# Kernel optimization log

Measured on AMD Instinct MI355X. Metric: run time of the kernel, lower is better.

## Reference

```python
import jax, jax.numpy as jnp
import numpy as np

B, T, I, H = 64, 2048, 64, 256


def setup_inputs() -> dict:
    key = jax.random.key(0)
    ks = jax.random.split(key, 7)
    s_ih = 1.0 / np.sqrt(H)
    return {
        "x": jax.random.normal(ks[0], (B, T, I), dtype=jnp.float32),
        "W_ih": jax.random.normal(ks[1], (H, I), dtype=jnp.float32) * s_ih,
        "W_hh": jax.random.normal(ks[2], (H, H), dtype=jnp.float32) * s_ih,
        "b_ih": jax.random.normal(ks[3], (H,), dtype=jnp.float32) * s_ih,
        "b_hh": jax.random.normal(ks[4], (H,), dtype=jnp.float32) * s_ih,
        "W_fc": jax.random.normal(ks[5], (1, H), dtype=jnp.float32) * s_ih,
        "b_fc": jax.random.normal(ks[6], (1,), dtype=jnp.float32) * s_ih,
    }


def reference(x, W_ih, W_hh, b_ih, b_hh, W_fc, b_fc):
    # Precompute input projection for all timesteps: [B,T,H]
    pre = jnp.einsum('bti,hi->bth', x, W_ih) + b_ih + b_hh
    pre_t = jnp.swapaxes(pre, 0, 1)  # [T,B,H]

    def step(h, p_t):
        h_new = jnp.tanh(p_t + h @ W_hh.T)
        return h_new, h_new

    h0 = jnp.zeros((x.shape[0], W_hh.shape[0]), dtype=x.dtype)
    _, hs = jax.lax.scan(step, h0, pre_t)  # hs: [T,B,H]
    out = jnp.swapaxes(hs, 0, 1)  # [B,T,H]
    return out @ W_fc.T + b_fc  # [B,T,1]
```

## Files before the change

### kernel.cpp

```cpp
#include <hip/hip_runtime.h>

#define BB 64
#define TT 2048
#define II 64
#define HH 256

typedef __fp16 h2_t __attribute__((ext_vector_type(2)));
typedef __fp16 h8_t __attribute__((ext_vector_type(8)));

#define H2(i) __builtin_bit_cast(h2_t, (i))
#define I32(h) __builtin_bit_cast(int, (h))

#if __has_builtin(__builtin_amdgcn_fdot2)
#define FDOT2(a, b, c) __builtin_amdgcn_fdot2((a), (b), (c), false)
#else
__device__ __forceinline__ float FDOT2(h2_t a, h2_t b, float c) {
    return fmaf((float)a[0], (float)b[0], fmaf((float)a[1], (float)b[1], c));
}
#endif

__device__ __forceinline__ float ftanh(float x) {
    float e = __expf(2.0f * x);
    return 1.0f - 2.0f * __builtin_amdgcn_rcpf(e + 1.0f);
}

template <int CTRL>
__device__ __forceinline__ float dpp_add(float v) {
    int s = __builtin_amdgcn_update_dpp(0, __float_as_int(v), CTRL, 0xF, 0xF, true);
    return v + __int_as_float(s);
}
template <int CTRL>
__device__ __forceinline__ float dpp_get(float v) {
    int s = __builtin_amdgcn_update_dpp(0, __float_as_int(v), CTRL, 0xF, 0xF, true);
    return __int_as_float(s);
}
template <int PAT>
__device__ __forceinline__ float swz_get(float v) {
    return __int_as_float(__builtin_amdgcn_ds_swizzle(__float_as_int(v), PAT));
}

__device__ __forceinline__ float mrg4(float a, float b, int lane) {
    float t = (lane & 4) ? b : a;
    float u = (lane & 4) ? a : b;
    return t + swz_get<0x101F>(u);
}
__device__ __forceinline__ float mrg2(float a, float b, int lane) {
    float t = (lane & 2) ? b : a;
    float u = (lane & 2) ? a : b;
    return t + dpp_get<0x4E>(u);
}
__device__ __forceinline__ float mrg1(float a, float b, int lane) {
    float t = (lane & 1) ? b : a;
    float u = (lane & 1) ? a : b;
    return t + dpp_get<0xB1>(u);
}

__launch_bounds__(256, 1)
__global__ void rnn_fused(const float* __restrict__ x,
                          const float* __restrict__ W_ih,
                          const float* __restrict__ W_hh,
                          const float* __restrict__ b_ih,
                          const float* __restrict__ b_hh,
                          const float* __restrict__ W_fc,
                          const float* __restrict__ b_fc,
                          float* __restrict__ out) {
    __shared__ __align__(16) __fp16 hbuf[2][320];
    __shared__ float part[TT + 1][8];

    const int tid  = threadIdx.x;
    const int b    = blockIdx.x;
    const int lane = tid & 63;
    const int w    = tid >> 6;
    const int o    = lane >> 3;
    const int q    = lane & 7;

    int whh_i[8][16];
    int wih_i[8][4];
#pragma unroll
    for (int r = 0; r < 8; ++r) {
        const int t_r = w * 64 + o * 8 + r;
        const float4* wr = (const float4*)(W_hh + t_r * HH + q * 32);
#pragma unroll
        for (int jv = 0; jv < 8; ++jv) {
            const float4 wv = wr[jv];
            whh_i[r][jv * 2 + 0] = I32(__builtin_amdgcn_cvt_pkrtz(wv.x, wv.y));
            whh_i[r][jv * 2 + 1] = I32(__builtin_amdgcn_cvt_pkrtz(wv.z, wv.w));
        }
        const float4* wi = (const float4*)(W_ih + t_r * II + q * 8);
        const float4 wa = wi[0], wb = wi[1];
        wih_i[r][0] = I32(__builtin_amdgcn_cvt_pkrtz(wa.x, wa.y));
        wih_i[r][1] = I32(__builtin_amdgcn_cvt_pkrtz(wa.z, wa.w));
        wih_i[r][2] = I32(__builtin_amdgcn_cvt_pkrtz(wb.x, wb.y));
        wih_i[r][3] = I32(__builtin_amdgcn_cvt_pkrtz(wb.z, wb.w));
    }
#pragma unroll
    for (int j = 0; j < 128; ++j) asm volatile("" : "+v"(((int*)whh_i)[j]));
#pragma unroll
    for (int j = 0; j < 32; ++j) asm volatile("" : "+v"(((int*)wih_i)[j]));

    const int myrow = w * 64 + lane;
    const float bias = b_ih[myrow] + b_hh[myrow];
    const float wfc  = W_fc[myrow];
    const float bfc  = b_fc[0];

    for (int idx = tid; idx < 2 * 320; idx += 256) ((__fp16*)hbuf)[idx] = (__fp16)0.0f;
    __syncthreads();

    const float* xbase = x + (size_t)b * TT * II + q * 8;
    float* outb = out + (size_t)b * TT;

    const int hoff = (w * 2 + (lane >> 5)) * 80 + (lane & 31) * 2;
    __fp16* hw0 = (__fp16*)((char*)&hbuf[0][0] + hoff);
    __fp16* hw1 = (__fp16*)((char*)&hbuf[1][0] + hoff);
    const h8_t* hp0 = (const h8_t*)((const char*)&hbuf[0][0] + q * 80);
    const h8_t* hp1 = (const h8_t*)((const char*)&hbuf[1][0] + q * 80);

    h2_t xc[4];
    float4 sAa, sAc, sBa, sBc;
    {
        const float4* xp = (const float4*)(xbase);
        const float4 a = xp[0], c = xp[1];
        xc[0] = __builtin_amdgcn_cvt_pkrtz(a.x, a.y);
        xc[1] = __builtin_amdgcn_cvt_pkrtz(a.z, a.w);
        xc[2] = __builtin_amdgcn_cvt_pkrtz(c.x, c.y);
        xc[3] = __builtin_amdgcn_cvt_pkrtz(c.z, c.w);
        const float4* x1 = (const float4*)(xbase + II);
        sAa = x1[0]; sAc = x1[1];
        const float4* x2 = (const float4*)(xbase + 2 * II);
        sBa = x2[0]; sBc = x2[1];
    }

    float hn_prev = 0.0f;

#define STEP(IDX, HPIN, HWOUT, SA, SC)                                         \
    {                                                                          \
          \
        const h8_t hv0 = (HPIN)[0], hv1 = (HPIN)[1];                           \
        const h8_t hv2 = (HPIN)[2], hv3 = (HPIN)[3];                           \
           \
        {                                                                      \
            float c = hn_prev * wfc;                                           \
            c = dpp_add<0xB1>(c);                                      \
            c = dpp_add<0x4E>(c);                                      \
            c = dpp_add<0x141>(c);                \
            c = dpp_add<0x140>(c);                     \
            c = dpp_add<0x142>(c);    \
            if ((lane & 31) == 16) part[IDX][w * 2 + (lane >> 5)] = c;         \
        }                                                                      \
                 \
        float a0 = 0, a1 = 0, a2 = 0, a3 = 0, a4 = 0, a5 = 0, a6 = 0, a7 = 0;  \
        _Pragma("unroll")                                                      \
        for (int jv = 0; jv < 4; ++jv) {                                       \
            const h8_t hv = (jv == 0) ? hv0 : (jv == 1) ? hv1                  \
                          : (jv == 2) ? hv2 : hv3;                             \
            _Pragma("unroll")                                                  \
            for (int e = 0; e < 4; ++e) {                                      \
                const h2_t he = (e == 0) ? __builtin_shufflevector(hv, hv, 0, 1) \
                              : (e == 1) ? __builtin_shufflevector(hv, hv, 2, 3) \
                              : (e == 2) ? __builtin_shufflevector(hv, hv, 4, 5) \
                                         : __builtin_shufflevector(hv, hv, 6, 7); \
                const int j = jv * 4 + e;                                      \
                a0 = FDOT2(H2(whh_i[0][j]), he, a0);                           \
                a1 = FDOT2(H2(whh_i[1][j]), he, a1);                           \
                a2 = FDOT2(H2(whh_i[2][j]), he, a2);                           \
                a3 = FDOT2(H2(whh_i[3][j]), he, a3);                           \
                a4 = FDOT2(H2(whh_i[4][j]), he, a4);                           \
                a5 = FDOT2(H2(whh_i[5][j]), he, a5);                           \
                a6 = FDOT2(H2(whh_i[6][j]), he, a6);                           \
                a7 = FDOT2(H2(whh_i[7][j]), he, a7);                           \
            }                                                                  \
        }                                                                      \
        _Pragma("unroll")                                                      \
        for (int e = 0; e < 4; ++e) {                                          \
            a0 = FDOT2(H2(wih_i[0][e]), xc[e], a0);                            \
            a1 = FDOT2(H2(wih_i[1][e]), xc[e], a1);                            \
            a2 = FDOT2(H2(wih_i[2][e]), xc[e], a2);                            \
            a3 = FDOT2(H2(wih_i[3][e]), xc[e], a3);                            \
            a4 = FDOT2(H2(wih_i[4][e]), xc[e], a4);                            \
            a5 = FDOT2(H2(wih_i[5][e]), xc[e], a5);                            \
            a6 = FDOT2(H2(wih_i[6][e]), xc[e], a6);                            \
            a7 = FDOT2(H2(wih_i[7][e]), xc[e], a7);                            \
        }                                                                      \
         \
        xc[0] = __builtin_amdgcn_cvt_pkrtz((SA).x, (SA).y);                    \
        xc[1] = __builtin_amdgcn_cvt_pkrtz((SA).z, (SA).w);                    \
        xc[2] = __builtin_amdgcn_cvt_pkrtz((SC).x, (SC).y);                    \
        xc[3] = __builtin_amdgcn_cvt_pkrtz((SC).z, (SC).w);                    \
        {                                                                      \
            const int rn = ((IDX) + 3 < TT) ? ((IDX) + 3) : (TT - 1);          \
            const float4* xp = (const float4*)(xbase + rn * II);               \
            (SA) = xp[0]; (SC) = xp[1];                                        \
        }                                                                      \
         \
        const float A0 = mrg4(a0, a4, lane);                                   \
        const float A1 = mrg4(a1, a5, lane);                                   \
        const float A2 = mrg4(a2, a6, lane);                                   \
        const float A3 = mrg4(a3, a7, lane);                                   \
        const float B0 = mrg2(A0, A2, lane);                                   \
        const float B1 = mrg2(A1, A3, lane);                                   \
        const float C0 = mrg1(B0, B1, lane);                                   \
        const float hn = ftanh(C0 + bias);                                     \
        (HWOUT)[0] = (__fp16)hn;                                               \
        hn_prev = hn;                                                          \
           \
                             \
        asm volatile("s_waitcnt lgkmcnt(0)\n\ts_barrier" ::: "memory");        \
    }

    for (int ib = 0; ib < TT; ib += 2) {
        STEP(ib, hp0, hw1, sAa, sAc)
        STEP(ib + 1, hp1, hw0, sBa, sBc)
    }
#undef STEP

    {
        float c = hn_prev * wfc;
        c = dpp_add<0xB1>(c);
        c = dpp_add<0x4E>(c);
        c = dpp_add<0x141>(c);
        c = dpp_add<0x140>(c);
        c = dpp_add<0x142>(c);
        if ((lane & 31) == 16) part[TT][w * 2 + (lane >> 5)] = c;
    }
    __syncthreads();

    for (int i = tid; i < TT; i += 256) {
        const float4* pp = (const float4*)&part[i + 1][0];
        const float4 s0 = pp[0], s1 = pp[1];
        outb[i] = s0.x + s0.y + s0.z + s0.w + s1.x + s1.y + s1.z + s1.w + bfc;
    }
}

extern "C" void kernel_launch(void* const* d_in, const int* in_sizes, int n_in,
                              void* d_out, int out_size, void* d_ws, size_t ws_size,
                              hipStream_t stream) {
    const float* x    = (const float*)d_in[0];
    const float* W_ih = (const float*)d_in[1];
    const float* W_hh = (const float*)d_in[2];
    const float* b_ih = (const float*)d_in[3];
    const float* b_hh = (const float*)d_in[4];
    const float* W_fc = (const float*)d_in[5];
    const float* b_fc = (const float*)d_in[6];
    float* out = (float*)d_out;

    rnn_fused<<<BB, 256, 0, stream>>>(x, W_ih, W_hh, b_ih, b_hh, W_fc, b_fc, out);
}
```

Baseline: 1.171 ms.

## Split recurrent rows across 512 threads to halve per-thread dot-product work

The block grows from 256 to 512 threads, so each thread now holds 4 weight rows instead of 8. That halves the serial FDOT2 chain per timestep and the register footprint. The cross-lane reduction loses one merge stage, and each row ends up computed by two lanes, so the output-projection weight is halved to avoid double counting. The cost is 8 waves per barrier, duplicated tanh work, and wider per-step partial sums in LDS.

New measurement: 1.245 ms. 1.06x slower.

```diff
diff --git a/kernel.cpp b/kernel.cpp
--- a/kernel.cpp
+++ b/kernel.cpp
@@ -4,6 +4,7 @@
 #define TT 2048
 #define II 64
 #define HH 256
+#define NTHR 512
 
 typedef __fp16 h2_t __attribute__((ext_vector_type(2)));
 typedef __fp16 h8_t __attribute__((ext_vector_type(8)));
@@ -49,13 +50,8 @@
     float u = (lane & 2) ? a : b;
     return t + dpp_get<0x4E>(u);
 }
-__device__ __forceinline__ float mrg1(float a, float b, int lane) {
-    float t = (lane & 1) ? b : a;
-    float u = (lane & 1) ? a : b;
-    return t + dpp_get<0xB1>(u);
-}
-
-__launch_bounds__(256, 1)
+
+__launch_bounds__(NTHR, 2)
 __global__ void rnn_fused(const float* __restrict__ x,
                           const float* __restrict__ W_ih,
                           const float* __restrict__ W_hh,
@@ -65,26 +61,26 @@
                           const float* __restrict__ b_fc,
                           float* __restrict__ out) {
     __shared__ __align__(16) __fp16 hbuf[2][320];
-    __shared__ float part[TT + 1][8];
+    __shared__ float part[TT + 1][16];
 
     const int tid  = threadIdx.x;
     const int b    = blockIdx.x;
     const int lane = tid & 63;
-    const int w    = tid >> 6;
+    const int wv   = tid >> 6;
     const int o    = lane >> 3;
     const int q    = lane & 7;
 
-    int whh_i[8][16];
-    int wih_i[8][4];
-#pragma unroll
-    for (int r = 0; r < 8; ++r) {
-        const int t_r = w * 64 + o * 8 + r;
+    int whh_i[4][16];
+    int wih_i[4][4];
+#pragma unroll
+    for (int r = 0; r < 4; ++r) {
+        const int t_r = wv * 32 + o * 4 + r;
         const float4* wr = (const float4*)(W_hh + t_r * HH + q * 32);
 #pragma unroll
         for (int jv = 0; jv < 8; ++jv) {
-            const float4 wv = wr[jv];
-            whh_i[r][jv * 2 + 0] = I32(__builtin_amdgcn_cvt_pkrtz(wv.x, wv.y));
-            whh_i[r][jv * 2 + 1] = I32(__builtin_amdgcn_cvt_pkrtz(wv.z, wv.w));
+            const float4 wv4 = wr[jv];
+            whh_i[r][jv * 2 + 0] = I32(__builtin_amdgcn_cvt_pkrtz(wv4.x, wv4.y));
+            whh_i[r][jv * 2 + 1] = I32(__builtin_amdgcn_cvt_pkrtz(wv4.z, wv4.w));
         }
         const float4* wi = (const float4*)(W_ih + t_r * II + q * 8);
         const float4 wa = wi[0], wb = wi[1];
@@ -94,22 +90,23 @@
         wih_i[r][3] = I32(__builtin_amdgcn_cvt_pkrtz(wb.z, wb.w));
     }
 #pragma unroll
-    for (int j = 0; j < 128; ++j) asm volatile("" : "+v"(((int*)whh_i)[j]));
-#pragma unroll
-    for (int j = 0; j < 32; ++j) asm volatile("" : "+v"(((int*)wih_i)[j]));
-
-    const int myrow = w * 64 + lane;
+    for (int j = 0; j < 64; ++j) asm volatile("" : "+v"(((int*)whh_i)[j]));
+#pragma unroll
+    for (int j = 0; j < 16; ++j) asm volatile("" : "+v"(((int*)wih_i)[j]));
+
+    const int r_own = (lane >> 1) & 3;
+    const int myrow = wv * 32 + o * 4 + r_own;
     const float bias = b_ih[myrow] + b_hh[myrow];
-    const float wfc  = W_fc[myrow];
+    const float wfc  = W_fc[myrow] * 0.5f;
     const float bfc  = b_fc[0];
 
-    for (int idx = tid; idx < 2 * 320; idx += 256) ((__fp16*)hbuf)[idx] = (__fp16)0.0f;
+    for (int idx = tid; idx < 2 * 320; idx += NTHR) ((__fp16*)hbuf)[idx] = (__fp16)0.0f;
     __syncthreads();
 
     const float* xbase = x + (size_t)b * TT * II + q * 8;
     float* outb = out + (size_t)b * TT;
 
-    const int hoff = (w * 2 + (lane >> 5)) * 80 + (lane & 31) * 2;
+    const int hoff = wv * 80 + (myrow & 31) * 2;
     __fp16* hw0 = (__fp16*)((char*)&hbuf[0][0] + hoff);
     __fp16* hw1 = (__fp16*)((char*)&hbuf[1][0] + hoff);
     const h8_t* hp0 = (const h8_t*)((const char*)&hbuf[0][0] + q * 80);
@@ -145,10 +142,10 @@
             c = dpp_add<0x141>(c);                \
             c = dpp_add<0x140>(c);                     \
             c = dpp_add<0x142>(c);    \
-            if ((lane & 31) == 16) part[IDX][w * 2 + (lane >> 5)] = c;         \
+            if ((lane & 31) == 16) part[IDX][wv * 2 + (lane >> 5)] = c;        \
         }                                                                      \
                  \
-        float a0 = 0, a1 = 0, a2 = 0, a3 = 0, a4 = 0, a5 = 0, a6 = 0, a7 = 0;  \
+        float a0 = 0, a1 = 0, a2 = 0, a3 = 0;                                  \
         _Pragma("unroll")                                                      \
         for (int jv = 0; jv < 4; ++jv) {                                       \
             const h8_t hv = (jv == 0) ? hv0 : (jv == 1) ? hv1                  \
@@ -164,10 +161,6 @@
                 a1 = FDOT2(H2(whh_i[1][j]), he, a1);                           \
                 a2 = FDOT2(H2(whh_i[2][j]), he, a2);                           \
                 a3 = FDOT2(H2(whh_i[3][j]), he, a3);                           \
-                a4 = FDOT2(H2(whh_i[4][j]), he, a4);                           \
-                a5 = FDOT2(H2(whh_i[5][j]), he, a5);                           \
-                a6 = FDOT2(H2(whh_i[6][j]), he, a6);                           \
-                a7 = FDOT2(H2(whh_i[7][j]), he, a7);                           \
             }                                                                  \
         }                                                                      \
         _Pragma("unroll")                                                      \
@@ -176,10 +169,6 @@
             a1 = FDOT2(H2(wih_i[1][e]), xc[e], a1);                            \
             a2 = FDOT2(H2(wih_i[2][e]), xc[e], a2);                            \
             a3 = FDOT2(H2(wih_i[3][e]), xc[e], a3);                            \
-            a4 = FDOT2(H2(wih_i[4][e]), xc[e], a4);                            \
-            a5 = FDOT2(H2(wih_i[5][e]), xc[e], a5);                            \
-            a6 = FDOT2(H2(wih_i[6][e]), xc[e], a6);                            \
-            a7 = FDOT2(H2(wih_i[7][e]), xc[e], a7);                            \
         }                                                                      \
          \
         xc[0] = __builtin_amdgcn_cvt_pkrtz((SA).x, (SA).y);                    \
@@ -191,15 +180,13 @@
             const float4* xp = (const float4*)(xbase + rn * II);               \
             (SA) = xp[0]; (SC) = xp[1];                                        \
         }                                                                      \
-         \
-        const float A0 = mrg4(a0, a4, lane);                                   \
-        const float A1 = mrg4(a1, a5, lane);                                   \
-        const float A2 = mrg4(a2, a6, lane);                                   \
-        const float A3 = mrg4(a3, a7, lane);                                   \
-        const float B0 = mrg2(A0, A2, lane);                                   \
-        const float B1 = mrg2(A1, A3, lane);                                   \
-        const float C0 = mrg1(B0, B1, lane);                                   \
-        const float hn = ftanh(C0 + bias);                                     \
+                             \
+        const float M0 = mrg4(a0, a2, lane);                                   \
+        const float M1 = mrg4(a1, a3, lane);                                   \
+        const float C0 = mrg2(M0, M1, lane);                                   \
+        const float C  = C0 + dpp_get<0xB1>(C0);      \
+        const float hn = ftanh(C + bias);                                      \
+             \
         (HWOUT)[0] = (__fp16)hn;                                               \
         hn_prev = hn;                                                          \
            \
@@ -220,14 +207,15 @@
         c = dpp_add<0x141>(c);
         c = dpp_add<0x140>(c);
         c = dpp_add<0x142>(c);
-        if ((lane & 31) == 16) part[TT][w * 2 + (lane >> 5)] = c;
+        if ((lane & 31) == 16) part[TT][wv * 2 + (lane >> 5)] = c;
     }
     __syncthreads();
 
-    for (int i = tid; i < TT; i += 256) {
+    for (int i = tid; i < TT; i += NTHR) {
         const float4* pp = (const float4*)&part[i + 1][0];
-        const float4 s0 = pp[0], s1 = pp[1];
-        outb[i] = s0.x + s0.y + s0.z + s0.w + s1.x + s1.y + s1.z + s1.w + bfc;
+        const float4 s0 = pp[0], s1 = pp[1], s2 = pp[2], s3 = pp[3];
+        outb[i] = s0.x + s0.y + s0.z + s0.w + s1.x + s1.y + s1.z + s1.w +
+                  s2.x + s2.y + s2.z + s2.w + s3.x + s3.y + s3.z + s3.w + bfc;
     }
 }
 
@@ -243,5 +231,5 @@
     const float* b_fc = (const float*)d_in[6];
     float* out = (float*)d_out;
 
-    rnn_fused<<<BB, 256, 0, stream>>>(x, W_ih, W_hh, b_ih, b_hh, W_fc, b_fc, out);
-}
+    rnn_fused<<<BB, NTHR, 0, stream>>>(x, W_ih, W_hh, b_ih, b_hh, W_fc, b_fc, out);
+}
```

## Interleave h buffer layout, hoist input projection before recurrent dot, use DPP for merge

Applied to the files above, without the earlier changes.

Changes the shared hidden-state layout from padded 80-byte segments to a dense interleaved [4][64] layout, where each lane reads 16 bytes at stride 128, and reorders W_hh register loading to match. The input-projection dot products and the next x conversion and prefetch move ahead of the recurrent dot, so that work can overlap the LDS read latency of h. The ds_swizzle in the 4-lane merge is replaced with two DPP row-shift reads plus a select, keeping that step off LDS. Bank-conflict behaviour of the new layout and the extra DPP op both bear on the serial per-step latency.

Result: faster. 1.137 ms (-2.9%).

```diff
diff --git a/kernel.cpp b/kernel.cpp
--- a/kernel.cpp
+++ b/kernel.cpp
@@ -4,6 +4,7 @@
 #define TT 2048
 #define II 64
 #define HH 256
+#define NTHR 256
 
 typedef __fp16 h2_t __attribute__((ext_vector_type(2)));
 typedef __fp16 h8_t __attribute__((ext_vector_type(8)));
@@ -34,15 +35,13 @@
     int s = __builtin_amdgcn_update_dpp(0, __float_as_int(v), CTRL, 0xF, 0xF, true);
     return __int_as_float(s);
 }
-template <int PAT>
-__device__ __forceinline__ float swz_get(float v) {
-    return __int_as_float(__builtin_amdgcn_ds_swizzle(__float_as_int(v), PAT));
-}
 
 __device__ __forceinline__ float mrg4(float a, float b, int lane) {
     float t = (lane & 4) ? b : a;
     float u = (lane & 4) ? a : b;
-    return t + swz_get<0x101F>(u);
+    float r4  = dpp_get<0x124>(u);
+    float r12 = dpp_get<0x12C>(u);
+    return t + ((lane & 4) ? r4 : r12);
 }
 __device__ __forceinline__ float mrg2(float a, float b, int lane) {
     float t = (lane & 2) ? b : a;
@@ -55,7 +54,7 @@
     return t + dpp_get<0xB1>(u);
 }
 
-__launch_bounds__(256, 1)
+__launch_bounds__(NTHR, 1)
 __global__ void rnn_fused(const float* __restrict__ x,
                           const float* __restrict__ W_ih,
                           const float* __restrict__ W_hh,
@@ -64,7 +63,7 @@
                           const float* __restrict__ W_fc,
                           const float* __restrict__ b_fc,
                           float* __restrict__ out) {
-    __shared__ __align__(16) __fp16 hbuf[2][320];
+    __shared__ __align__(16) __fp16 hbuf[2][4][64];
     __shared__ float part[TT + 1][8];
 
     const int tid  = threadIdx.x;
@@ -79,12 +78,14 @@
 #pragma unroll
     for (int r = 0; r < 8; ++r) {
         const int t_r = w * 64 + o * 8 + r;
-        const float4* wr = (const float4*)(W_hh + t_r * HH + q * 32);
-#pragma unroll
-        for (int jv = 0; jv < 8; ++jv) {
-            const float4 wv = wr[jv];
-            whh_i[r][jv * 2 + 0] = I32(__builtin_amdgcn_cvt_pkrtz(wv.x, wv.y));
-            whh_i[r][jv * 2 + 1] = I32(__builtin_amdgcn_cvt_pkrtz(wv.z, wv.w));
+#pragma unroll
+        for (int c = 0; c < 4; ++c) {
+            const float4* wr = (const float4*)(W_hh + t_r * HH + c * 64 + q * 8);
+            const float4 wa = wr[0], wb = wr[1];
+            whh_i[r][c * 4 + 0] = I32(__builtin_amdgcn_cvt_pkrtz(wa.x, wa.y));
+            whh_i[r][c * 4 + 1] = I32(__builtin_amdgcn_cvt_pkrtz(wa.z, wa.w));
+            whh_i[r][c * 4 + 2] = I32(__builtin_amdgcn_cvt_pkrtz(wb.x, wb.y));
+            whh_i[r][c * 4 + 3] = I32(__builtin_amdgcn_cvt_pkrtz(wb.z, wb.w));
         }
         const float4* wi = (const float4*)(W_ih + t_r * II + q * 8);
         const float4 wa = wi[0], wb = wi[1];
@@ -103,17 +104,18 @@
     const float wfc  = W_fc[myrow];
     const float bfc  = b_fc[0];
 
-    for (int idx = tid; idx < 2 * 320; idx += 256) ((__fp16*)hbuf)[idx] = (__fp16)0.0f;
+    for (int idx = tid; idx < 2 * 256; idx += NTHR) ((__fp16*)hbuf)[idx] = (__fp16)0.0f;
     __syncthreads();
 
     const float* xbase = x + (size_t)b * TT * II + q * 8;
     float* outb = out + (size_t)b * TT;
 
-    const int hoff = (w * 2 + (lane >> 5)) * 80 + (lane & 31) * 2;
-    __fp16* hw0 = (__fp16*)((char*)&hbuf[0][0] + hoff);
-    __fp16* hw1 = (__fp16*)((char*)&hbuf[1][0] + hoff);
-    const h8_t* hp0 = (const h8_t*)((const char*)&hbuf[0][0] + q * 80);
-    const h8_t* hp1 = (const h8_t*)((const char*)&hbuf[1][0] + q * 80);
+    char* hb0 = (char*)&hbuf[0][0][0];
+    char* hb1 = (char*)&hbuf[1][0][0];
+    __fp16* hw0 = (__fp16*)(hb0 + w * 128 + lane * 2);
+    __fp16* hw1 = (__fp16*)(hb1 + w * 128 + lane * 2);
+    const char* hq0 = hb0 + q * 16;
+    const char* hq1 = hb1 + q * 16;
 
     h2_t xc[4];
     float4 sAa, sAc, sBa, sBc;
@@ -132,34 +134,66 @@
 
     float hn_prev = 0.0f;
 
-#define STEP(IDX, HPIN, HWOUT, SA, SC)                                         \
+#define STEP(IDX, HRD, HWOUT, SA, SC)                                          \
     {                                                                          \
-          \
-        const h8_t hv0 = (HPIN)[0], hv1 = (HPIN)[1];                           \
-        const h8_t hv2 = (HPIN)[2], hv3 = (HPIN)[3];                           \
+           \
+        const h8_t hv0 = *(const h8_t*)((HRD) + 0 * 128);                      \
+        const h8_t hv1 = *(const h8_t*)((HRD) + 1 * 128);                      \
+        const h8_t hv2 = *(const h8_t*)((HRD) + 2 * 128);                      \
+        const h8_t hv3 = *(const h8_t*)((HRD) + 3 * 128);                      \
            \
         {                                                                      \
-            float c = hn_prev * wfc;                                           \
-            c = dpp_add<0xB1>(c);                                      \
-            c = dpp_add<0x4E>(c);                                      \
-            c = dpp_add<0x141>(c);                \
-            c = dpp_add<0x140>(c);                     \
-            c = dpp_add<0x142>(c);    \
-            if ((lane & 31) == 16) part[IDX][w * 2 + (lane >> 5)] = c;         \
-        }                                                                      \
-                 \
-        float a0 = 0, a1 = 0, a2 = 0, a3 = 0, a4 = 0, a5 = 0, a6 = 0, a7 = 0;  \
+            float hc = hn_prev * wfc;                                          \
+            hc = dpp_add<0xB1>(hc);                                    \
+            hc = dpp_add<0x4E>(hc);                                    \
+            hc = dpp_add<0x141>(hc);                  \
+            hc = dpp_add<0x140>(hc);                   \
+            hc = dpp_add<0x142>(hc);       \
+            if ((lane & 31) == 16) part[IDX][w * 2 + (lane >> 5)] = hc;        \
+        }                                                                      \
+              \
+        float a0, a1, a2, a3, a4, a5, a6, a7;                                  \
+        a0 = FDOT2(H2(wih_i[0][0]), xc[0], 0.0f);                              \
+        a1 = FDOT2(H2(wih_i[1][0]), xc[0], 0.0f);                              \
+        a2 = FDOT2(H2(wih_i[2][0]), xc[0], 0.0f);                              \
+        a3 = FDOT2(H2(wih_i[3][0]), xc[0], 0.0f);                              \
+        a4 = FDOT2(H2(wih_i[4][0]), xc[0], 0.0f);                              \
+        a5 = FDOT2(H2(wih_i[5][0]), xc[0], 0.0f);                              \
+        a6 = FDOT2(H2(wih_i[6][0]), xc[0], 0.0f);                              \
+        a7 = FDOT2(H2(wih_i[7][0]), xc[0], 0.0f);                              \
         _Pragma("unroll")                                                      \
-        for (int jv = 0; jv < 4; ++jv) {                                       \
-            const h8_t hv = (jv == 0) ? hv0 : (jv == 1) ? hv1                  \
-                          : (jv == 2) ? hv2 : hv3;                             \
+        for (int e = 1; e < 4; ++e) {                                          \
+            a0 = FDOT2(H2(wih_i[0][e]), xc[e], a0);                            \
+            a1 = FDOT2(H2(wih_i[1][e]), xc[e], a1);                            \
+            a2 = FDOT2(H2(wih_i[2][e]), xc[e], a2);                            \
+            a3 = FDOT2(H2(wih_i[3][e]), xc[e], a3);                            \
+            a4 = FDOT2(H2(wih_i[4][e]), xc[e], a4);                            \
+            a5 = FDOT2(H2(wih_i[5][e]), xc[e], a5);                            \
+            a6 = FDOT2(H2(wih_i[6][e]), xc[e], a6);                            \
+            a7 = FDOT2(H2(wih_i[7][e]), xc[e], a7);                            \
+        }                                                                      \
+                        \
+        xc[0] = __builtin_amdgcn_cvt_pkrtz((SA).x, (SA).y);                    \
+        xc[1] = __builtin_amdgcn_cvt_pkrtz((SA).z, (SA).w);                    \
+        xc[2] = __builtin_amdgcn_cvt_pkrtz((SC).x, (SC).y);                    \
+        xc[3] = __builtin_amdgcn_cvt_pkrtz((SC).z, (SC).w);                    \
+        {                                                                      \
+            const int rn = ((IDX) + 3 < TT) ? ((IDX) + 3) : (TT - 1);          \
+            const float4* xp = (const float4*)(xbase + rn * II);               \
+            (SA) = xp[0]; (SC) = xp[1];                                        \
+        }                                                                      \
+             \
+        _Pragma("unroll")                                                      \
+        for (int c = 0; c < 4; ++c) {                                          \
+            const h8_t hv = (c == 0) ? hv0 : (c == 1) ? hv1                    \
+                          : (c == 2) ? hv2 : hv3;                              \
             _Pragma("unroll")                                                  \
             for (int e = 0; e < 4; ++e) {                                      \
                 const h2_t he = (e == 0) ? __builtin_shufflevector(hv, hv, 0, 1) \
                               : (e == 1) ? __builtin_shufflevector(hv, hv, 2, 3) \
                               : (e == 2) ? __builtin_shufflevector(hv, hv, 4, 5) \
                                          : __builtin_shufflevector(hv, hv, 6, 7); \
-                const int j = jv * 4 + e;                                      \
+                const int j = c * 4 + e;                                       \
                 a0 = FDOT2(H2(whh_i[0][j]), he, a0);                           \
                 a1 = FDOT2(H2(whh_i[1][j]), he, a1);                           \
                 a2 = FDOT2(H2(whh_i[2][j]), he, a2);                           \
@@ -170,28 +204,7 @@
                 a7 = FDOT2(H2(whh_i[7][j]), he, a7);                           \
             }                                                                  \
         }                                                                      \
-        _Pragma("unroll")                                                      \
-        for (int e = 0; e < 4; ++e) {                                          \
-            a0 = FDOT2(H2(wih_i[0][e]), xc[e], a0);                            \
-            a1 = FDOT2(H2(wih_i[1][e]), xc[e], a1);                            \
-            a2 = FDOT2(H2(wih_i[2][e]), xc[e], a2);                            \
-            a3 = FDOT2(H2(wih_i[3][e]), xc[e], a3);                            \
-            a4 = FDOT2(H2(wih_i[4][e]), xc[e], a4);                            \
-            a5 = FDOT2(H2(wih_i[5][e]), xc[e], a5);                            \
-            a6 = FDOT2(H2(wih_i[6][e]), xc[e], a6);                            \
-            a7 = FDOT2(H2(wih_i[7][e]), xc[e], a7);                            \
-        }                                                                      \
-         \
-        xc[0] = __builtin_amdgcn_cvt_pkrtz((SA).x, (SA).y);                    \
-        xc[1] = __builtin_amdgcn_cvt_pkrtz((SA).z, (SA).w);                    \
-        xc[2] = __builtin_amdgcn_cvt_pkrtz((SC).x, (SC).y);                    \
-        xc[3] = __builtin_amdgcn_cvt_pkrtz((SC).z, (SC).w);                    \
-        {                                                                      \
-            const int rn = ((IDX) + 3 < TT) ? ((IDX) + 3) : (TT - 1);          \
-            const float4* xp = (const float4*)(xbase + rn * II);               \
-            (SA) = xp[0]; (SC) = xp[1];                                        \
-        }                                                                      \
-         \
+                            \
         const float A0 = mrg4(a0, a4, lane);                                   \
         const float A1 = mrg4(a1, a5, lane);                                   \
         const float A2 = mrg4(a2, a6, lane);                                   \
@@ -202,29 +215,28 @@
         const float hn = ftanh(C0 + bias);                                     \
         (HWOUT)[0] = (__fp16)hn;                                               \
         hn_prev = hn;                                                          \
-           \
-                             \
+                   \
         asm volatile("s_waitcnt lgkmcnt(0)\n\ts_barrier" ::: "memory");        \
     }
 
     for (int ib = 0; ib < TT; ib += 2) {
-        STEP(ib, hp0, hw1, sAa, sAc)
-        STEP(ib + 1, hp1, hw0, sBa, sBc)
+        STEP(ib, hq0, hw1, sAa, sAc)
+        STEP(ib + 1, hq1, hw0, sBa, sBc)
     }
 #undef STEP
 
     {
-        float c = hn_prev * wfc;
-        c = dpp_add<0xB1>(c);
-        c = dpp_add<0x4E>(c);
-        c = dpp_add<0x141>(c);
-        c = dpp_add<0x140>(c);
-        c = dpp_add<0x142>(c);
-        if ((lane & 31) == 16) part[TT][w * 2 + (lane >> 5)] = c;
+        float hc = hn_prev * wfc;
+        hc = dpp_add<0xB1>(hc);
+        hc = dpp_add<0x4E>(hc);
+        hc = dpp_add<0x141>(hc);
+        hc = dpp_add<0x140>(hc);
+        hc = dpp_add<0x142>(hc);
+        if ((lane & 31) == 16) part[TT][w * 2 + (lane >> 5)] = hc;
     }
     __syncthreads();
 
-    for (int i = tid; i < TT; i += 256) {
+    for (int i = tid; i < TT; i += NTHR) {
         const float4* pp = (const float4*)&part[i + 1][0];
         const float4 s0 = pp[0], s1 = pp[1];
         outb[i] = s0.x + s0.y + s0.z + s0.w + s1.x + s1.y + s1.z + s1.w + bfc;
@@ -243,5 +255,5 @@
     const float* b_fc = (const float*)d_in[6];
     float* out = (float*)d_out;
 
-    rnn_fused<<<BB, 256, 0, stream>>>(x, W_ih, W_hh, b_ih, b_hh, W_fc, b_fc, out);
-}
+    rnn_fused<<<BB, NTHR, 0, stream>>>(x, W_ih, W_hh, b_ih, b_hh, W_fc, b_fc, out);
+}
```
